# Optimization experiments

Hardware: AMD Instinct MI355X
Metric: run time of the kernel (lower is better)

Reference implementation:

```python
import jax, jax.numpy as jnp
import numpy as np


def setup_inputs() -> dict:
    key = jax.random.key(0)
    k1, k2, k3 = jax.random.split(key, 3)
    RAW_NODES = 40962          # ico-6 sphere
    NUM_NODES = RAW_NODES * 4 - 6   # 163842, ico-7 sphere
    FEAT = 256
    x = jax.random.normal(k1, (RAW_NODES, FEAT), dtype=jnp.float32)
    max_index = jax.random.randint(k2, (RAW_NODES, FEAT), 0, 7, dtype=jnp.int64)
    neigh_orders = jax.random.randint(k3, (RAW_NODES * 7,), 0, NUM_NODES, dtype=jnp.int64)
    return {"x": x, "max_index": max_index, "neigh_orders": neigh_orders, "num_nodes": NUM_NODES}


def reference(x, max_index, neigh_orders, num_nodes):
    raw_nodes, feat_num = x.shape
    # column_ref[i, f] = i*7 + max_index[i, f]  (vectorized form of the python loop)
    column_ref = (jnp.arange(raw_nodes, dtype=max_index.dtype)[:, None] * 7 + max_index).reshape(-1)
    column_index = neigh_orders[column_ref]  # gather from neighborhood lookup table
    # row_index exactly as in the original: floor(linspace(0, feat_num, raw_nodes*feat_num)), last clamped
    row_index = np.floor(np.linspace(0.0, float(feat_num), num=raw_nodes * feat_num)).astype(np.int64)
    row_index[-1] = row_index[-1] - 1
    row_index = jnp.asarray(row_index)
    y = jnp.zeros((num_nodes, feat_num), dtype=x.dtype)
    # scatter: y[column_index, row_index] = x.view(-1)
    y = y.at[column_index, row_index].set(x.reshape(-1))
    return y
```

## Files before the change

kernel.cpp:

```cpp
#include <hip/hip_runtime.h>
#include <stdint.h>


#define FEAT 256
#define LOG2FEAT 8
#define BLOCK 256
#define BUILD_WGS 256
#define ZERO_WGS 1024
#define EPN 8

extern "C" __global__ __launch_bounds__(BLOCK)
void build_zero_kernel(const int*   __restrict__ mi,
                       const int*   __restrict__ neigh,
                       float*       __restrict__ out,
                       int*         __restrict__ T,
                       int2*        __restrict__ entries,
                       int total,
                       int out_elems)
{
    const int tid = threadIdx.x;

    if (blockIdx.x >= BUILD_WGS) {
        const int zid = blockIdx.x - BUILD_WGS;
        float4* out4 = (float4*)out;
        const int total4 = out_elems >> 2;
        const float4 z = make_float4(0.f, 0.f, 0.f, 0.f);
        for (int idx = zid * BLOCK + tid; idx < total4; idx += ZERO_WGS * BLOCK)
            out4[idx] = z;
        return;
    }

    const int lane      = tid & 63;
    const int wv        = (blockIdx.x * BLOCK + tid) >> 6;
    const int nwaves    = BUILD_WGS * (BLOCK / 64);
    const int raw_nodes = total >> LOG2FEAT;
    const int n_main    = raw_nodes * EPN;
    const unsigned tm1  = (unsigned)(total - 1);

    int p0 = 0, p1 = 0, p2 = 0, p3 = 0;
    if (wv < raw_nodes) {
        const int* mrow = mi + (wv << LOG2FEAT);
        p0 = mrow[lane]; p1 = mrow[64 + lane];
        p2 = mrow[128 + lane]; p3 = mrow[192 + lane];
    }

    for (int i = wv; i < raw_nodes; i += nwaves) {
        const int m0 = p0, m1 = p1, m2 = p2, m3 = p3;
        const int i_n = i + nwaves;
        if (i_n < raw_nodes) {
            const int* mrow = mi + (i_n << LOG2FEAT);
            p0 = mrow[lane]; p1 = mrow[64 + lane];
            p2 = mrow[128 + lane]; p3 = mrow[192 + lane];
        }

        const int kbase = i << LOG2FEAT;
        unsigned long long b[4][7];
        #pragma unroll
        for (int m = 0; m < 7; ++m) {
            b[0][m] = __ballot(m0 == m);
            b[1][m] = __ballot(m1 == m);
            b[2][m] = __ballot(m2 == m);
            b[3][m] = __ballot(m3 == m);
        }

        unsigned r_first = (((unsigned)kbase) << 8) / tm1;
        unsigned r_last  = (((unsigned)(kbase + FEAT - 1)) << 8) / tm1;
        if (r_last > 255u) r_last = 255u;
        const bool straddle = (r_last != r_first);
        unsigned fb = FEAT;
        if (straddle) fb = ((r_last * tm1 + 255u) >> 8) - (unsigned)kbase;

        unsigned long long g[4];
        #pragma unroll
        for (int j = 0; j < 4; ++j)
            g[j] = (fb >= (unsigned)(j + 1) * 64) ? ~0ull
                 : (fb <= (unsigned)j * 64)       ? 0ull
                 : ((1ull << (fb - (unsigned)j * 64)) - 1ull);

        int  m  = -1;
        bool hi = false;
        if (lane < 7)                                { m = lane;     hi = false; }
        else if (straddle && lane >= 8 && lane < 15) { m = lane - 8; hi = true;  }

        int2 ent = make_int2(0, 0);
        if (m >= 0) {
            int bestf = -1;
            #pragma unroll
            for (int j = 3; j >= 0; --j) {
                if (bestf < 0) {
                    unsigned long long s =
                        (m == 0) ? b[j][0] : (m == 1) ? b[j][1] :
                        (m == 2) ? b[j][2] : (m == 3) ? b[j][3] :
                        (m == 4) ? b[j][4] : (m == 5) ? b[j][5] : b[j][6];
                    unsigned long long t = s & (hi ? ~g[j] : g[j]);
                    if (t) bestf = j * 64 + 63 - __clzll(t);
                }
            }
            if (bestf >= 0) {
                const int k   = kbase + bestf;
                const int col = neigh[i * 7 + m];
                const int r   = hi ? (int)r_last : (int)r_first;
                ent = make_int2((col << LOG2FEAT) | r, k + 1);
                atomicMax(&T[ent.x], ent.y);
            }
        }
        if (lane < EPN)
            entries[(size_t)i * EPN + lane] = ent;
        if (straddle && lane >= 8 && lane < 8 + EPN)
            entries[(size_t)n_main + ((size_t)r_last - 1u) * EPN + (lane - 8)] = ent;
    }
}

extern "C" __global__ __launch_bounds__(256)
void value_kernel(int* __restrict__ out_i,
                  const float* __restrict__ x,
                  const int*  __restrict__ T,
                  const int2* __restrict__ entries,
                  int n_entries)
{
    for (int idx = blockIdx.x * 256 + threadIdx.x; idx < n_entries;
         idx += gridDim.x * 256) {
        const int2 e = entries[idx];
        if (e.y > 0 && T[e.x] == e.y)
            out_i[e.x] = __float_as_int(x[e.y - 1]);
    }
}

extern "C" void kernel_launch(void* const* d_in, const int* in_sizes, int n_in,
                              void* d_out, int out_size, void* d_ws, size_t ws_size,
                              hipStream_t stream) {
    const float* x     = (const float*)d_in[0];
    const int*   mi    = (const int*)d_in[1];
    const int*   neigh = (const int*)d_in[2];
    float*       out   = (float*)d_out;

    const int total     = in_sizes[0];
    const int out_elems = out_size;
    const int raw_nodes = total >> LOG2FEAT;
    const int n_entries = raw_nodes * EPN + 255 * EPN;

    int*  T       = (int*)d_ws;
    int2* entries = (int2*)((char*)d_ws + (size_t)out_elems * sizeof(int));

    build_zero_kernel<<<dim3(BUILD_WGS + ZERO_WGS), dim3(BLOCK), 0, stream>>>(
        mi, neigh, out, T, entries, total, out_elems);
    value_kernel<<<dim3(512), dim3(256), 0, stream>>>(
        (int*)out, x, T, entries, n_entries);
}
```

Baseline: 332.1 us.

## Pack value into 64-bit atomicMax key and add nontemporal zeroing stores

The scatter winner selection now uses a 64-bit atomicMax on a key that packs the source index (with a tag prefix) in the high word and the float bits of x in the low word. The resolve pass can then read the winning value straight from the table instead of comparing stamps and gathering from x. The output zeroing and the max_index reads switch to nontemporal stores and loads, and the resolve grid grows. In exchange the workspace table doubles in size and the scattered atomics become 64-bit, which may make each random atomic more expensive.

```diff
diff --git a/kernel.cpp b/kernel.cpp
--- a/kernel.cpp
+++ b/kernel.cpp
@@ -8,13 +8,17 @@
 #define BUILD_WGS 256
 #define ZERO_WGS 1024
 #define EPN 8
+#define TAG_PREFIX 0xC000000000000000ull
+
+typedef float nt_float4 __attribute__((ext_vector_type(4)));
 
 extern "C" __global__ __launch_bounds__(BLOCK)
-void build_zero_kernel(const int*   __restrict__ mi,
+void build_zero_kernel(const float* __restrict__ x,
+                       const int*   __restrict__ mi,
                        const int*   __restrict__ neigh,
                        float*       __restrict__ out,
-                       int*         __restrict__ T,
-                       int2*        __restrict__ entries,
+                       unsigned long long* __restrict__ T64,
+                       int*         __restrict__ entries,
                        int total,
                        int out_elems)
 {
@@ -22,11 +26,11 @@
 
     if (blockIdx.x >= BUILD_WGS) {
         const int zid = blockIdx.x - BUILD_WGS;
-        float4* out4 = (float4*)out;
+        nt_float4* out4 = (nt_float4*)out;
         const int total4 = out_elems >> 2;
-        const float4 z = make_float4(0.f, 0.f, 0.f, 0.f);
+        const nt_float4 z = {0.f, 0.f, 0.f, 0.f};
         for (int idx = zid * BLOCK + tid; idx < total4; idx += ZERO_WGS * BLOCK)
-            out4[idx] = z;
+            __builtin_nontemporal_store(z, &out4[idx]);
         return;
     }
 
@@ -40,8 +44,10 @@
     int p0 = 0, p1 = 0, p2 = 0, p3 = 0;
     if (wv < raw_nodes) {
         const int* mrow = mi + (wv << LOG2FEAT);
-        p0 = mrow[lane]; p1 = mrow[64 + lane];
-        p2 = mrow[128 + lane]; p3 = mrow[192 + lane];
+        p0 = __builtin_nontemporal_load(&mrow[lane]);
+        p1 = __builtin_nontemporal_load(&mrow[64 + lane]);
+        p2 = __builtin_nontemporal_load(&mrow[128 + lane]);
+        p3 = __builtin_nontemporal_load(&mrow[192 + lane]);
     }
 
     for (int i = wv; i < raw_nodes; i += nwaves) {
@@ -49,8 +55,10 @@
         const int i_n = i + nwaves;
         if (i_n < raw_nodes) {
             const int* mrow = mi + (i_n << LOG2FEAT);
-            p0 = mrow[lane]; p1 = mrow[64 + lane];
-            p2 = mrow[128 + lane]; p3 = mrow[192 + lane];
+            p0 = __builtin_nontemporal_load(&mrow[lane]);
+            p1 = __builtin_nontemporal_load(&mrow[64 + lane]);
+            p2 = __builtin_nontemporal_load(&mrow[128 + lane]);
+            p3 = __builtin_nontemporal_load(&mrow[192 + lane]);
         }
 
         const int kbase = i << LOG2FEAT;
@@ -82,7 +90,7 @@
         if (lane < 7)                                { m = lane;     hi = false; }
         else if (straddle && lane >= 8 && lane < 15) { m = lane - 8; hi = true;  }
 
-        int2 ent = make_int2(0, 0);
+        int myslot = -1;
         if (m >= 0) {
             int bestf = -1;
             #pragma unroll
@@ -100,29 +108,32 @@
                 const int k   = kbase + bestf;
                 const int col = neigh[i * 7 + m];
                 const int r   = hi ? (int)r_last : (int)r_first;
-                ent = make_int2((col << LOG2FEAT) | r, k + 1);
-                atomicMax(&T[ent.x], ent.y);
+                myslot = (col << LOG2FEAT) | r;
+                const unsigned vb = (unsigned)__float_as_int(x[k]);
+                const unsigned long long packed =
+                    TAG_PREFIX | ((unsigned long long)(k + 1) << 32) | vb;
+                atomicMax(&T64[myslot], packed);
             }
         }
         if (lane < EPN)
-            entries[(size_t)i * EPN + lane] = ent;
+            entries[(size_t)i * EPN + lane] = (lane < 7) ? myslot : -1;
         if (straddle && lane >= 8 && lane < 8 + EPN)
-            entries[(size_t)n_main + ((size_t)r_last - 1u) * EPN + (lane - 8)] = ent;
+            entries[(size_t)n_main + ((size_t)r_last - 1u) * EPN + (lane - 8)] =
+                (lane < 15) ? myslot : -1;
     }
 }
 
 extern "C" __global__ __launch_bounds__(256)
-void value_kernel(int* __restrict__ out_i,
-                  const float* __restrict__ x,
-                  const int*  __restrict__ T,
-                  const int2* __restrict__ entries,
-                  int n_entries)
+void resolve_kernel(int* __restrict__ out_i,
+                    const unsigned long long* __restrict__ T64,
+                    const int* __restrict__ entries,
+                    int n_entries)
 {
     for (int idx = blockIdx.x * 256 + threadIdx.x; idx < n_entries;
          idx += gridDim.x * 256) {
-        const int2 e = entries[idx];
-        if (e.y > 0 && T[e.x] == e.y)
-            out_i[e.x] = __float_as_int(x[e.y - 1]);
+        const int s = entries[idx];
+        if (s >= 0)
+            out_i[s] = (int)T64[s];
     }
 }
 
@@ -139,11 +150,11 @@
     const int raw_nodes = total >> LOG2FEAT;
     const int n_entries = raw_nodes * EPN + 255 * EPN;
 
-    int*  T       = (int*)d_ws;
-    int2* entries = (int2*)((char*)d_ws + (size_t)out_elems * sizeof(int));
+    unsigned long long* T64 = (unsigned long long*)d_ws;
+    int* entries = (int*)((char*)d_ws + (size_t)out_elems * sizeof(unsigned long long));
 
     build_zero_kernel<<<dim3(BUILD_WGS + ZERO_WGS), dim3(BLOCK), 0, stream>>>(
-        mi, neigh, out, T, entries, total, out_elems);
-    value_kernel<<<dim3(512), dim3(256), 0, stream>>>(
-        (int*)out, x, T, entries, n_entries);
+        x, mi, neigh, out, T64, entries, total, out_elems);
+    resolve_kernel<<<dim3(1312), dim3(256), 0, stream>>>(
+        (int*)out, T64, entries, n_entries);
 }
```

After: 336.7 us. About the same (+1.4%).
